# Kernel optimization log

Measured on AMD Instinct MI355X. Metric: run time of the kernel, lower is better.

The kernel has to match this reference:

```python
import jax, jax.numpy as jnp
import numpy as np

B, S, D_IN, D_OUT = 4, 2048, 4096, 4096

def setup_inputs() -> dict:
    key = jax.random.key(0)
    k1, k2, k3 = jax.random.split(key, 3)
    x = jax.random.normal(k1, (B, S, D_IN), dtype=jnp.float32)
    quantized_weight = jax.random.randint(k2, (D_OUT, D_IN), 0, 127, dtype=jnp.int32)
    weight_zero_point = jax.random.randint(k3, (1,), 0, 10, dtype=jnp.int32)
    weight_scale = jnp.full((1,), 0.01, dtype=jnp.float32)
    bias = jnp.zeros((D_OUT,), dtype=jnp.float32)
    return {"x": x, "quantized_weight": quantized_weight,
            "weight_zero_point": weight_zero_point,
            "weight_scale": weight_scale, "bias": bias}

def reference(x, quantized_weight, weight_zero_point, weight_scale, bias):
    # dequantize_weight: (q - zp) * scale, then F.linear(x, W, b) = x @ W.T + b
    w = (quantized_weight.astype(jnp.float32)
         - weight_zero_point.astype(jnp.float32)) * weight_scale  # [D_OUT, D_IN]
    return jnp.einsum('bsi,oi->bso', x, w) + bias
```

## Files before the change

### kernel.cpp

```cpp
#include <hip/hip_runtime.h>


typedef __bf16 bf16x8 __attribute__((ext_vector_type(8)));
typedef float  f32x4  __attribute__((ext_vector_type(4)));


__global__ __launch_bounds__(256) void cvt_x_bf16(
    const float4* __restrict__ x, uint4* __restrict__ o, int n8) {
  int i = blockIdx.x * 256 + threadIdx.x;
  if (i >= n8) return;
  float4 a = x[2 * i];
  float4 b = x[2 * i + 1];
  union { __bf16 h[8]; uint4 u; } r;
  r.h[0] = (__bf16)a.x; r.h[1] = (__bf16)a.y;
  r.h[2] = (__bf16)a.z; r.h[3] = (__bf16)a.w;
  r.h[4] = (__bf16)b.x; r.h[5] = (__bf16)b.y;
  r.h[6] = (__bf16)b.z; r.h[7] = (__bf16)b.w;
  o[i] = r.u;
}

__global__ __launch_bounds__(256) void cvt_w_bf16(
    const int4* __restrict__ q, const int* __restrict__ zp,
    uint4* __restrict__ o, int n8) {
  int i = blockIdx.x * 256 + threadIdx.x;
  if (i >= n8) return;
  int z = zp[0];
  int4 a = q[2 * i];
  int4 b = q[2 * i + 1];
  union { __bf16 h[8]; uint4 u; } r;
  r.h[0] = (__bf16)(float)(a.x - z); r.h[1] = (__bf16)(float)(a.y - z);
  r.h[2] = (__bf16)(float)(a.z - z); r.h[3] = (__bf16)(float)(a.w - z);
  r.h[4] = (__bf16)(float)(b.x - z); r.h[5] = (__bf16)(float)(b.y - z);
  r.h[6] = (__bf16)(float)(b.z - z); r.h[7] = (__bf16)(float)(b.w - z);
  o[i] = r.u;
}


#define SLOT_A(d, h) ((((d) * 2 + (h)) << 14))
#define SLOT_B(d, h) ((1 << 16) + (((d) * 2 + (h)) << 14))

#define STAGE(gbase, ldsOff, h, s)                                            \
  do {                                                                        \
    const char* g_ = (gbase) + (size_t)(h) * 128 * K2 + (size_t)(s) * 128;    \
    __builtin_amdgcn_global_load_lds(                                         \
        (const __attribute__((address_space(1))) void*)(g_),                  \
        (__attribute__((address_space(3))) void*)(smem + (ldsOff) + wave * 2048), \
        16, 0, 0);                                                            \
    __builtin_amdgcn_global_load_lds(                                         \
        (const __attribute__((address_space(1))) void*)(g_ + 64),             \
        (__attribute__((address_space(3))) void*)(smem + (ldsOff) + wave * 2048 + 1024), \
        16, 0, 0);                                                            \
  } while (0)

#define LOAD_AF(d, qm)                                                        \
  do {                                                                        \
    _Pragma("unroll") for (int mf = 0; mf < 4; ++mf)                          \
    _Pragma("unroll") for (int kh = 0; kh < 2; ++kh)                          \
        af[mf][kh] = *(const bf16x8*)(smem + SLOT_A(d, qm) +                  \
            (((wr * 4 + mf) * 2 + kh) << 10) + innerOff);                     \
  } while (0)

#define LOAD_BF(dst, d, qn)                                                   \
  do {                                                                        \
    _Pragma("unroll") for (int nf = 0; nf < 2; ++nf)                          \
    _Pragma("unroll") for (int kh = 0; kh < 2; ++kh)                          \
        dst[nf][kh] = *(const bf16x8*)(smem + SLOT_B(d, qn) +                 \
            (((wc * 2 + nf) * 2 + kh) << 10) + innerOff);                     \
  } while (0)

#define MFMA_QUAD(qm, qn, BFR)                                                \
  do {                                                                        \
    __builtin_amdgcn_s_setprio(1);                                            \
    _Pragma("unroll") for (int kh = 0; kh < 2; ++kh)                          \
    _Pragma("unroll") for (int mf = 0; mf < 4; ++mf)                          \
    _Pragma("unroll") for (int nf = 0; nf < 2; ++nf)                          \
        acc[qm][qn][mf][nf] = __builtin_amdgcn_mfma_f32_16x16x32_bf16(        \
            af[mf][kh], BFR[nf][kh], acc[qm][qn][mf][nf], 0, 0, 0);           \
    __builtin_amdgcn_s_setprio(0);                                            \
  } while (0)

#define TILE_BODY(t, d, e)                                                    \
  do {                                                                        \
                                               \
    LOAD_AF(d, 0);                                                            \
    LOAD_BF(bf0, d, 0);                                                       \
    if ((t) + 1 < nt) STAGE(Abase, SLOT_A(e, 1), 1, (t) + 1);                 \
    MFMA_QUAD(0, 0, bf0);                                                     \
    __builtin_amdgcn_s_barrier();                                             \
                                                \
    LOAD_BF(bf1, d, 1);                                                       \
    if ((t) + 2 < nt) STAGE(Abase, SLOT_A(d, 0), 0, (t) + 2);                 \
    MFMA_QUAD(0, 1, bf1);                                                     \
    __builtin_amdgcn_s_barrier();                                             \
                                                \
    LOAD_AF(d, 1);                                                            \
    if ((t) + 2 < nt) STAGE(Bbase, SLOT_B(d, 0), 0, (t) + 2);                 \
    MFMA_QUAD(1, 1, bf1);                                                     \
    __builtin_amdgcn_s_barrier();                                             \
                                                \
    if ((t) + 2 < nt) STAGE(Bbase, SLOT_B(d, 1), 1, (t) + 2);                 \
    MFMA_QUAD(1, 0, bf0);                                                     \
    if ((t) + 2 < nt) { asm volatile("s_waitcnt vmcnt(6)"); }                 \
    else if ((t) + 1 < nt) { asm volatile("s_waitcnt vmcnt(0)"); }            \
    __builtin_amdgcn_s_barrier();                                             \
  } while (0)

__global__ __launch_bounds__(512, 2) void gemm256(
    const __bf16* __restrict__ A, const __bf16* __restrict__ Bw,
    const float* __restrict__ scale, const float* __restrict__ bias,
    float* __restrict__ C) {
  extern __shared__ char smem[];

  constexpr int M = 8192, N = 4096, K = 4096;
  constexpr size_t K2 = (size_t)K * 2;
  (void)M;

  const int tid  = threadIdx.x;
  const int wave = tid >> 6;
  const int lane = tid & 63;
  const int fr   = lane & 15;
  const int quad = lane >> 4;
  const int wr   = wave >> 2;
  const int wc   = wave & 3;

  const int nwg = gridDim.x;
  const int cpx = nwg >> 3;
  const int swzid = ((int)blockIdx.x & 7) * cpx + ((int)blockIdx.x >> 3);
  const int nbx = N >> 8;
  const int bx = swzid % nbx;
  const int by = swzid / nbx;

  const int rowLane = wave * 16 + (lane >> 2);
  const int colLane = ((lane & 3) << 4) ^ (((lane >> 3) & 3) << 4);
  const char* Abase = (const char*)A  + (size_t)(by * 256 + rowLane) * K2 + colLane;
  const char* Bbase = (const char*)Bw + (size_t)(bx * 256 + rowLane) * K2 + colLane;

  const int innerOff = (fr << 6) | ((quad << 4) ^ (((fr >> 1) & 3) << 4));

  f32x4 acc[2][2][4][2] = {};
  bf16x8 af[4][2], bf0[2][2], bf1[2][2];

  const int nt = K >> 6;

  STAGE(Abase, SLOT_A(0, 0), 0, 0);
  STAGE(Abase, SLOT_A(0, 1), 1, 0);
  STAGE(Bbase, SLOT_B(0, 0), 0, 0);
  STAGE(Bbase, SLOT_B(0, 1), 1, 0);
  STAGE(Abase, SLOT_A(1, 0), 0, 1);
  STAGE(Bbase, SLOT_B(1, 0), 0, 1);
  STAGE(Bbase, SLOT_B(1, 1), 1, 1);
  asm volatile("s_waitcnt vmcnt(6)");
  __builtin_amdgcn_s_barrier();

  for (int tt = 0; tt < nt; tt += 2) {
    TILE_BODY(tt, 0, 1);
    TILE_BODY(tt + 1, 1, 0);
  }

  const float s = scale[0];
#pragma unroll
  for (int qm = 0; qm < 2; ++qm)
#pragma unroll
    for (int mf = 0; mf < 4; ++mf) {
      const int row0 = by * 256 + qm * 128 + wr * 64 + mf * 16 + quad * 4;
#pragma unroll
      for (int qn = 0; qn < 2; ++qn)
#pragma unroll
        for (int nf = 0; nf < 2; ++nf) {
          const int col = bx * 256 + qn * 128 + wc * 32 + nf * 16 + fr;
          const float bv = bias[col];
          float* cp = C + (size_t)row0 * N + col;
#pragma unroll
          for (int r = 0; r < 4; ++r)
            cp[(size_t)r * N] = s * acc[qm][qn][mf][nf][r] + bv;
        }
    }
}


extern "C" void kernel_launch(void* const* d_in, const int* in_sizes, int n_in,
                              void* d_out, int out_size, void* d_ws, size_t ws_size,
                              hipStream_t stream) {
  const int M = 8192, N = 4096, K = 4096;

  const float* x    = (const float*)d_in[0];
  const int*   qw   = (const int*)d_in[1];
  const int*   zp   = (const int*)d_in[2];
  const float* sc   = (const float*)d_in[3];
  const float* bias = (const float*)d_in[4];
  float* out = (float*)d_out;

  __bf16* x_bf = (__bf16*)d_ws;
  __bf16* w_bf = (__bf16*)((char*)d_ws + (size_t)M * K * sizeof(__bf16));

  {
    int n8 = (M * K) / 8;
    cvt_x_bf16<<<n8 / 256, 256, 0, stream>>>((const float4*)x, (uint4*)x_bf, n8);
  }
  {
    int n8 = (N * K) / 8;
    cvt_w_bf16<<<n8 / 256, 256, 0, stream>>>((const int4*)qw, zp, (uint4*)w_bf, n8);
  }

  static bool attr_set = false;
  if (!attr_set) {
    hipFuncSetAttribute((const void*)gemm256,
                        hipFuncAttributeMaxDynamicSharedMemorySize, 131072);
    attr_set = true;
  }
  gemm256<<<dim3(512), dim3(512), 131072, stream>>>(x_bf, w_bf, sc, bias, out);
}
```

Baseline: 482.8 us.

## Restructure GEMM main loop into k-half phases with register double-buffered fragments

The tile body is reorganized from four quadrant phases over full K into four phases split by k-half, using ping-pong A/B register banks so LDS fragment reads for the next phase overlap the current MFMAs. Barriers per tile drop from four to two, global-to-LDS staging is regrouped (A and B halves staged together, whole tile t+1 preloaded in the prologue), and the last two iterations are peeled to remove runtime bounds checks. This aims to cut synchronization and LDS-latency stalls, at the cost of more live registers and tighter reliance on correct waitcnt ordering.

```diff
diff --git a/kernel.cpp b/kernel.cpp
--- a/kernel.cpp
+++ b/kernel.cpp
@@ -52,57 +52,53 @@
         16, 0, 0);                                                            \
   } while (0)
 
-#define LOAD_AF(d, qm)                                                        \
+#define LOAD_A(bank, d, qm, kh)                                               \
   do {                                                                        \
     _Pragma("unroll") for (int mf = 0; mf < 4; ++mf)                          \
-    _Pragma("unroll") for (int kh = 0; kh < 2; ++kh)                          \
-        af[mf][kh] = *(const bf16x8*)(smem + SLOT_A(d, qm) +                  \
-            (((wr * 4 + mf) * 2 + kh) << 10) + innerOff);                     \
-  } while (0)
-
-#define LOAD_BF(dst, d, qn)                                                   \
-  do {                                                                        \
-    _Pragma("unroll") for (int nf = 0; nf < 2; ++nf)                          \
-    _Pragma("unroll") for (int kh = 0; kh < 2; ++kh)                          \
-        dst[nf][kh] = *(const bf16x8*)(smem + SLOT_B(d, qn) +                 \
-            (((wc * 2 + nf) * 2 + kh) << 10) + innerOff);                     \
-  } while (0)
-
-#define MFMA_QUAD(qm, qn, BFR)                                                \
+        bank[mf] = *(const bf16x8*)(smem + SLOT_A(d, qm) +                    \
+            (((wr * 4 + mf) * 2 + (kh)) << 10) + innerOff);                   \
+  } while (0)
+
+#define LOAD_B(bank, d, kh)                                                   \
+  do {                                                                        \
+    _Pragma("unroll") for (int j = 0; j < 4; ++j)                             \
+        bank[j] = *(const bf16x8*)(smem + SLOT_B(d, (j >> 1)) +               \
+            (((wc * 2 + (j & 1)) * 2 + (kh)) << 10) + innerOff);              \
+  } while (0)
+
+#define MFMA_PH(qm, AF, BF)                                                   \
   do {                                                                        \
     __builtin_amdgcn_s_setprio(1);                                            \
-    _Pragma("unroll") for (int kh = 0; kh < 2; ++kh)                          \
     _Pragma("unroll") for (int mf = 0; mf < 4; ++mf)                          \
-    _Pragma("unroll") for (int nf = 0; nf < 2; ++nf)                          \
-        acc[qm][qn][mf][nf] = __builtin_amdgcn_mfma_f32_16x16x32_bf16(        \
-            af[mf][kh], BFR[nf][kh], acc[qm][qn][mf][nf], 0, 0, 0);           \
+    _Pragma("unroll") for (int j = 0; j < 4; ++j)                             \
+        acc[qm][j >> 1][mf][j & 1] = __builtin_amdgcn_mfma_f32_16x16x32_bf16( \
+            AF[mf], BF[j], acc[qm][j >> 1][mf][j & 1], 0, 0, 0);              \
     __builtin_amdgcn_s_setprio(0);                                            \
   } while (0)
 
-#define TILE_BODY(t, d, e)                                                    \
-  do {                                                                        \
-                                               \
-    LOAD_AF(d, 0);                                                            \
-    LOAD_BF(bf0, d, 0);                                                       \
-    if ((t) + 1 < nt) STAGE(Abase, SLOT_A(e, 1), 1, (t) + 1);                 \
-    MFMA_QUAD(0, 0, bf0);                                                     \
+#define TILE_K(t, d, e, FULL, PRE)                                            \
+  do {                                                                        \
+                                                                      \
+    LOAD_A(afB, d, 1, 0);                                                     \
+    MFMA_PH(0, afA, bfA);                                                     \
+                                                                      \
+    LOAD_A(afA, d, 0, 1);                                                     \
+    LOAD_B(bfB, d, 1);                                                        \
+    MFMA_PH(1, afB, bfA);                                                     \
     __builtin_amdgcn_s_barrier();                                             \
-                                                \
-    LOAD_BF(bf1, d, 1);                                                       \
-    if ((t) + 2 < nt) STAGE(Abase, SLOT_A(d, 0), 0, (t) + 2);                 \
-    MFMA_QUAD(0, 1, bf1);                                                     \
+                                                                      \
+    LOAD_A(afB, d, 1, 1);                                                     \
+    if (FULL) { STAGE(Abase, SLOT_A(d, 0), 0, (t) + 2);                       \
+                STAGE(Bbase, SLOT_B(d, 0), 0, (t) + 2); }                     \
+    MFMA_PH(0, afA, bfB);                                                     \
+    if (FULL)     { asm volatile("s_waitcnt vmcnt(4)"); }                     \
+    else if (PRE) { asm volatile("s_waitcnt vmcnt(0)"); }                     \
     __builtin_amdgcn_s_barrier();                                             \
-                                                \
-    LOAD_AF(d, 1);                                                            \
-    if ((t) + 2 < nt) STAGE(Bbase, SLOT_B(d, 0), 0, (t) + 2);                 \
-    MFMA_QUAD(1, 1, bf1);                                                     \
-    __builtin_amdgcn_s_barrier();                                             \
-                                                \
-    if ((t) + 2 < nt) STAGE(Bbase, SLOT_B(d, 1), 1, (t) + 2);                 \
-    MFMA_QUAD(1, 0, bf0);                                                     \
-    if ((t) + 2 < nt) { asm volatile("s_waitcnt vmcnt(6)"); }                 \
-    else if ((t) + 1 < nt) { asm volatile("s_waitcnt vmcnt(0)"); }            \
-    __builtin_amdgcn_s_barrier();                                             \
+                                                                      \
+    if (PRE) { LOAD_A(afA, e, 0, 0); LOAD_B(bfA, e, 0); }                     \
+    if (FULL) { STAGE(Abase, SLOT_A(d, 1), 1, (t) + 2);                       \
+                STAGE(Bbase, SLOT_B(d, 1), 1, (t) + 2); }                     \
+    MFMA_PH(1, afB, bfB);                                                     \
   } while (0)
 
 __global__ __launch_bounds__(512, 2) void gemm256(
@@ -111,9 +107,8 @@
     float* __restrict__ C) {
   extern __shared__ char smem[];
 
-  constexpr int M = 8192, N = 4096, K = 4096;
+  constexpr int N = 4096, K = 4096;
   constexpr size_t K2 = (size_t)K * 2;
-  (void)M;
 
   const int tid  = threadIdx.x;
   const int wave = tid >> 6;
@@ -138,24 +133,30 @@
   const int innerOff = (fr << 6) | ((quad << 4) ^ (((fr >> 1) & 3) << 4));
 
   f32x4 acc[2][2][4][2] = {};
-  bf16x8 af[4][2], bf0[2][2], bf1[2][2];
+  bf16x8 afA[4], afB[4], bfA[4], bfB[4];
 
   const int nt = K >> 6;
+  (void)nt;
 
   STAGE(Abase, SLOT_A(0, 0), 0, 0);
+  STAGE(Bbase, SLOT_B(0, 0), 0, 0);
   STAGE(Abase, SLOT_A(0, 1), 1, 0);
-  STAGE(Bbase, SLOT_B(0, 0), 0, 0);
   STAGE(Bbase, SLOT_B(0, 1), 1, 0);
   STAGE(Abase, SLOT_A(1, 0), 0, 1);
   STAGE(Bbase, SLOT_B(1, 0), 0, 1);
+  STAGE(Abase, SLOT_A(1, 1), 1, 1);
   STAGE(Bbase, SLOT_B(1, 1), 1, 1);
-  asm volatile("s_waitcnt vmcnt(6)");
+  asm volatile("s_waitcnt vmcnt(8)");
   __builtin_amdgcn_s_barrier();
-
-  for (int tt = 0; tt < nt; tt += 2) {
-    TILE_BODY(tt, 0, 1);
-    TILE_BODY(tt + 1, 1, 0);
-  }
+  LOAD_A(afA, 0, 0, 0);
+  LOAD_B(bfA, 0, 0);
+
+  for (int tt = 0; tt < 62; tt += 2) {
+    TILE_K(tt,     0, 1, 1, 1);
+    TILE_K(tt + 1, 1, 0, 1, 1);
+  }
+  TILE_K(62, 0, 1, 0, 1);
+  TILE_K(63, 1, 0, 0, 0);
 
   const float s = scale[0];
 #pragma unroll
```

After: 506.9 us. +5.0%, slower.

## Cut GEMM main-loop barriers from four to two per K tile and peel tail

Applied to the files above, without the earlier changes.

Restructures the bf16 GEMM tile body so each 64-wide K step runs two MFMA quads per phase with only two barriers instead of four. The later-tile prefetches are regrouped into one burst with adjusted vmcnt waits, and the loop is peeled so the last two tiles skip the runtime bounds checks. The aim is less barrier stall and fewer branches per iteration. In exchange, more global loads are in flight at once and the vmcnt counts must match the new issue order exactly, or the kernel will read shared memory before it is filled.

```diff
diff --git a/kernel.cpp b/kernel.cpp
--- a/kernel.cpp
+++ b/kernel.cpp
@@ -79,29 +79,26 @@
     __builtin_amdgcn_s_setprio(0);                                            \
   } while (0)
 
-#define TILE_BODY(t, d, e)                                                    \
-  do {                                                                        \
-                                               \
+#define TILE2(t, d, e, FULL, PRE)                                             \
+  do {                                                                        \
+                                                    \
     LOAD_AF(d, 0);                                                            \
     LOAD_BF(bf0, d, 0);                                                       \
-    if ((t) + 1 < nt) STAGE(Abase, SLOT_A(e, 1), 1, (t) + 1);                 \
+    if (PRE) STAGE(Abase, SLOT_A(e, 1), 1, (t) + 1);                          \
+    LOAD_BF(bf1, d, 1);                                                       \
     MFMA_QUAD(0, 0, bf0);                                                     \
+    MFMA_QUAD(0, 1, bf1);                                                     \
+    asm volatile("s_waitcnt vmcnt(8)");                                       \
     __builtin_amdgcn_s_barrier();                                             \
-                                                \
-    LOAD_BF(bf1, d, 1);                                                       \
-    if ((t) + 2 < nt) STAGE(Abase, SLOT_A(d, 0), 0, (t) + 2);                 \
-    MFMA_QUAD(0, 1, bf1);                                                     \
-    __builtin_amdgcn_s_barrier();                                             \
-                                                \
+                                                    \
     LOAD_AF(d, 1);                                                            \
-    if ((t) + 2 < nt) STAGE(Bbase, SLOT_B(d, 0), 0, (t) + 2);                 \
+    if (FULL) { STAGE(Abase, SLOT_A(d, 0), 0, (t) + 2);                       \
+                STAGE(Bbase, SLOT_B(d, 0), 0, (t) + 2);                       \
+                STAGE(Bbase, SLOT_B(d, 1), 1, (t) + 2); }                     \
     MFMA_QUAD(1, 1, bf1);                                                     \
-    __builtin_amdgcn_s_barrier();                                             \
-                                                \
-    if ((t) + 2 < nt) STAGE(Bbase, SLOT_B(d, 1), 1, (t) + 2);                 \
     MFMA_QUAD(1, 0, bf0);                                                     \
-    if ((t) + 2 < nt) { asm volatile("s_waitcnt vmcnt(6)"); }                 \
-    else if ((t) + 1 < nt) { asm volatile("s_waitcnt vmcnt(0)"); }            \
+    if (FULL) { asm volatile("s_waitcnt vmcnt(8)"); }                         \
+    else      { asm volatile("s_waitcnt vmcnt(0)"); }                         \
     __builtin_amdgcn_s_barrier();                                             \
   } while (0)
 
@@ -111,9 +108,8 @@
     float* __restrict__ C) {
   extern __shared__ char smem[];
 
-  constexpr int M = 8192, N = 4096, K = 4096;
+  constexpr int N = 4096, K = 4096;
   constexpr size_t K2 = (size_t)K * 2;
-  (void)M;
 
   const int tid  = threadIdx.x;
   const int wave = tid >> 6;
@@ -141,21 +137,24 @@
   bf16x8 af[4][2], bf0[2][2], bf1[2][2];
 
   const int nt = K >> 6;
+  (void)nt;
 
   STAGE(Abase, SLOT_A(0, 0), 0, 0);
-  STAGE(Abase, SLOT_A(0, 1), 1, 0);
   STAGE(Bbase, SLOT_B(0, 0), 0, 0);
   STAGE(Bbase, SLOT_B(0, 1), 1, 0);
+  STAGE(Abase, SLOT_A(0, 1), 1, 0);
   STAGE(Abase, SLOT_A(1, 0), 0, 1);
   STAGE(Bbase, SLOT_B(1, 0), 0, 1);
   STAGE(Bbase, SLOT_B(1, 1), 1, 1);
-  asm volatile("s_waitcnt vmcnt(6)");
+  asm volatile("s_waitcnt vmcnt(8)");
   __builtin_amdgcn_s_barrier();
 
-  for (int tt = 0; tt < nt; tt += 2) {
-    TILE_BODY(tt, 0, 1);
-    TILE_BODY(tt + 1, 1, 0);
-  }
+  for (int tt = 0; tt < 62; tt += 2) {
+    TILE2(tt,     0, 1, 1, 1);
+    TILE2(tt + 1, 1, 0, 1, 1);
+  }
+  TILE2(62, 0, 1, 0, 1);
+  TILE2(63, 1, 0, 0, 0);
 
   const float s = scale[0];
 #pragma unroll
```

Result: no change. 480.9 us (-0.4%).
